# Optimization experiments

Hardware: AMD Instinct MI355X
Metric: run time of the kernel (lower is better)

Reference implementation:

```python
import jax, jax.numpy as jnp
import numpy as np

N_NODES = 50000


def _gcn_edges(edge_index, n):
    # add self loops, then symmetric GCN normalization D^-1/2 (A+I) D^-1/2
    loop = jnp.arange(n, dtype=edge_index.dtype)
    src = jnp.concatenate([edge_index[0], loop])
    dst = jnp.concatenate([edge_index[1], loop])
    deg = jax.ops.segment_sum(jnp.ones_like(src, dtype=jnp.float32), dst, num_segments=n)
    dinv = jnp.where(deg > 0, jax.lax.rsqrt(deg), 0.0)
    norm = dinv[src] * dinv[dst]
    return src, dst, norm


def _encoder(x, edge_index, w1, b1, w2, b2, w3, b3, n):
    src, dst, norm = _gcn_edges(edge_index, n)

    def prop(h):
        # sparse spmm: scatter-add of normalized gathered source features
        return jax.ops.segment_sum(h[src] * norm[:, None], dst, num_segments=n)

    def layer(h, w, b):
        # powers [0,1,2]: incrementally apply adjacency, linear per power, concat
        outs, cur = [], h
        for p in range(w.shape[0]):
            if p > 0:
                cur = prop(cur)
            outs.append(cur @ w[p] + b[p])
        return jnp.tanh(jnp.concatenate(outs, axis=-1))

    h = layer(x, w1, b1)
    h = layer(h, w2, b2)
    return layer(h, w3, b3)


def setup_inputs() -> dict:
    key = jax.random.key(0)
    ks = jax.random.split(key, 16)
    n, e, d = N_NODES, 800000, 256
    inp = {
        "x": jax.random.normal(ks[0], (n, d), dtype=jnp.float32),
        "edge_index": jax.random.randint(ks[1], (2, e), 0, n, dtype=jnp.int64),
    }
    dims = [(d, 64), (192, 64), (192, 64)]
    i = 2
    for enc in ("out", "in"):
        for li, (din, dout) in enumerate(dims, start=1):
            s = 1.0 / np.sqrt(din)
            inp[f"w{enc}{li}"] = jax.random.uniform(ks[i], (3, din, dout), jnp.float32, -s, s); i += 1
            inp[f"b{enc}{li}"] = jax.random.uniform(ks[i], (3, dout), jnp.float32, -s, s); i += 1
    return inp


def reference(x, edge_index, wout1, bout1, wout2, bout2, wout3, bout3,
              win1, bin1, win2, bin2, win3, bin3):
    n = x.shape[0]
    zout = _encoder(x, edge_index, wout1, bout1, wout2, bout2, wout3, bout3, n)
    zin = _encoder(x, edge_index[::-1], win1, bin1, win2, bin2, win3, bin3, n)
    return (zout, zin)
```

## Files before the change

### kernel.cpp

```cpp
#include <hip/hip_runtime.h>
#include <hip/hip_bf16.h>

#define NN 50000
#define EE 800000
#define NTILES 782
#define NB 391

typedef __bf16 bf16x8 __attribute__((ext_vector_type(8)));
typedef unsigned short us8 __attribute__((ext_vector_type(8)));
typedef float f32x4 __attribute__((ext_vector_type(4)));

__device__ __forceinline__ unsigned short f2bf(float f) {
  unsigned u = __float_as_uint(f);
  u += 0x7FFFu + ((u >> 16) & 1u);
  return (unsigned short)(u >> 16);
}
__device__ __forceinline__ float bflo(unsigned u) { return __uint_as_float(u << 16); }
__device__ __forceinline__ float bfhi(unsigned u) { return __uint_as_float(u & 0xFFFF0000u); }
__device__ __forceinline__ float bf2f(unsigned short h) { return __uint_as_float(((unsigned)h) << 16); }
__device__ __forceinline__ float fast_tanh(float x) {
  float e = __expf(2.0f * x);
  return 1.0f - 2.0f / (e + 1.0f);
}


__global__ __launch_bounds__(256) void k_hist(const int* __restrict__ ei, int* __restrict__ bCnt) {
  __shared__ int h[2 * NB];
  for (int i = threadIdx.x; i < 2 * NB; i += 256) h[i] = 0;
  __syncthreads();
  int base = blockIdx.x * 2048;
#pragma unroll
  for (int j = 0; j < 8; ++j) {
    int e = base + j * 256 + threadIdx.x;
    if (e < EE) {
      int s = ei[e], d = ei[EE + e];
      atomicAdd(&h[d >> 7], 1);
      atomicAdd(&h[NB + (s >> 7)], 1);
    }
  }
  __syncthreads();
  for (int i = threadIdx.x; i < 2 * NB; i += 256) {
    int c = h[i];
    if (c) atomicAdd(&bCnt[i], c);
  }
}

__global__ __launch_bounds__(512) void k_bscan(const int* __restrict__ bCnt,
                                               int* __restrict__ bOff, int* __restrict__ bCur) {
  __shared__ int sd[512];
  int z = blockIdx.x, t = threadIdx.x;
  sd[t] = (t < NB) ? bCnt[z * NB + t] : 0;
  __syncthreads();
  for (int o = 1; o < 512; o <<= 1) {
    int v = (t >= o) ? sd[t - o] : 0;
    __syncthreads();
    sd[t] += v;
    __syncthreads();
  }
  int ex = (t > 0) ? sd[t - 1] : 0;
  if (t < NB) { bOff[z * (NB + 1) + t] = ex; bCur[z * NB + t] = ex; }
  if (t == NB) bOff[z * (NB + 1) + NB] = ex;
}

__global__ __launch_bounds__(256) void k_scatter(const int* __restrict__ ei,
                                                 int* __restrict__ bCur,
                                                 unsigned* __restrict__ binA,
                                                 unsigned* __restrict__ binB) {
  __shared__ int h[2 * NB];
  for (int i = threadIdx.x; i < 2 * NB; i += 256) h[i] = 0;
  __syncthreads();
  int base = blockIdx.x * 2048;
  int s[8], d[8], la[8], lb[8];
#pragma unroll
  for (int j = 0; j < 8; ++j) {
    int e = base + j * 256 + threadIdx.x;
    d[j] = -1;
    if (e < EE) {
      s[j] = ei[e]; d[j] = ei[EE + e];
      la[j] = atomicAdd(&h[d[j] >> 7], 1);
      lb[j] = atomicAdd(&h[NB + (s[j] >> 7)], 1);
    }
  }
  __syncthreads();
  for (int i = threadIdx.x; i < 2 * NB; i += 256) {
    int c = h[i];
    if (c) h[i] = atomicAdd(&bCur[i], c);
  }
  __syncthreads();
#pragma unroll
  for (int j = 0; j < 8; ++j) {
    if (d[j] >= 0) {
      int pa = h[d[j] >> 7] + la[j];
      binA[pa] = ((unsigned)s[j] << 7) | (unsigned)(d[j] & 127);
      int pb = h[NB + (s[j] >> 7)] + lb[j];
      binB[pb] = ((unsigned)d[j] << 7) | (unsigned)(s[j] & 127);
    }
  }
}

__global__ __launch_bounds__(256) void k_build(const unsigned* __restrict__ binA,
                                               const unsigned* __restrict__ binB,
                                               const int* __restrict__ bOff,
                                               int* __restrict__ rpA, int* __restrict__ rpB,
                                               int* __restrict__ colA, int* __restrict__ colB,
                                               float* __restrict__ dinvA, float* __restrict__ dinvB) {
  int z = blockIdx.y, b = blockIdx.x, t = threadIdx.x;
  const unsigned* bin = z ? binB : binA;
  int* rp = z ? rpB : rpA;
  int* col = z ? colB : colA;
  float* dinv = z ? dinvB : dinvA;

  int e0 = bOff[z * (NB + 1) + b], e1 = bOff[z * (NB + 1) + b + 1];

  __shared__ int cnt[128];
  __shared__ int scn[128];
  __shared__ int cur[128];
  if (t < 128) cnt[t] = 0;
  __syncthreads();
  for (int e = e0 + t; e < e1; e += 256) atomicAdd(&cnt[bin[e] & 127], 1);
  __syncthreads();
  if (t < 128) scn[t] = cnt[t];
  __syncthreads();
  for (int o = 1; o < 128; o <<= 1) {
    int v = (t < 128 && t >= o) ? scn[t - o] : 0;
    __syncthreads();
    if (t < 128) scn[t] += v;
    __syncthreads();
  }
  if (t < 128) {
    int ex = scn[t] - cnt[t];
    cur[t] = ex;
    int node = b * 128 + t;
    if (node <= NN) rp[node] = e0 + ex;
    if (node < NN) dinv[node] = rsqrtf((float)(cnt[t] + 1));
  }
  __syncthreads();
  for (int e = e0 + t; e < e1; e += 256) {
    unsigned p = bin[e];
    int pos = e0 + atomicAdd(&cur[p & 127], 1);
    col[pos] = (int)(p >> 7);
  }
}


template<int K, bool F32IN>
__global__ __launch_bounds__(256) void k_gemm(const void* __restrict__ in0, const void* __restrict__ in1,
                                              const float* __restrict__ W0, const float* __restrict__ W1,
                                              unsigned short* __restrict__ Z0, unsigned short* __restrict__ Z1) {
  constexpr int KS = K / 32;
  constexpr int KP = K + 8;
  __shared__ unsigned short A_lds[64 * KP];

  int z = blockIdx.y;
  const void* Ain = z ? in1 : in0;
  const float* W = z ? W1 : W0;
  unsigned short* Zo = z ? Z1 : Z0;

  int t = threadIdx.x;
  int lane = t & 63, wv = t >> 6;
  int nloc = lane & 15, quad = lane >> 4;

  bf16x8 b[3][KS];
#pragma unroll
  for (int nt = 0; nt < 3; ++nt) {
    int ncol = wv * 48 + nt * 16 + nloc;
    const float* wp = W + (ncol >> 6) * (K * 64) + (ncol & 63);
#pragma unroll
    for (int ks = 0; ks < KS; ++ks) {
      int kb = ks * 32 + quad * 8;
      us8 u;
#pragma unroll
      for (int i = 0; i < 8; ++i) u[i] = f2bf(wp[(kb + i) * 64]);
      b[nt][ks] = __builtin_bit_cast(bf16x8, u);
    }
  }

  for (int bm = blockIdx.x; bm < NTILES; bm += gridDim.x) {
    int m0 = bm * 64;
    __syncthreads();
#pragma unroll
    for (int it = 0; it < KS; ++it) {
      int c = it * 256 + t;
      int row = c / (K / 8);
      int kc  = c % (K / 8);
      int gr = m0 + row;
      us8 val;
      if (F32IN) {
        float4 v0 = make_float4(0, 0, 0, 0), v1 = make_float4(0, 0, 0, 0);
        if (gr < NN) {
          const float* Af = (const float*)Ain + (size_t)gr * K + kc * 8;
          v0 = *(const float4*)(Af);
          v1 = *(const float4*)(Af + 4);
        }
        val[0] = f2bf(v0.x); val[1] = f2bf(v0.y); val[2] = f2bf(v0.z); val[3] = f2bf(v0.w);
        val[4] = f2bf(v1.x); val[5] = f2bf(v1.y); val[6] = f2bf(v1.z); val[7] = f2bf(v1.w);
      } else {
        if (gr < NN) val = *(const us8*)((const unsigned short*)Ain + (size_t)gr * K + kc * 8);
        else         val = (us8)0;
      }
      *(us8*)(&A_lds[row * KP + kc * 8]) = val;
    }
    __syncthreads();

    f32x4 acc[4][3];
#pragma unroll
    for (int mt = 0; mt < 4; ++mt)
#pragma unroll
      for (int nt = 0; nt < 3; ++nt) acc[mt][nt] = (f32x4){0.f, 0.f, 0.f, 0.f};

#pragma unroll
    for (int ks = 0; ks < KS; ++ks) {
      bf16x8 a[4];
#pragma unroll
      for (int mt = 0; mt < 4; ++mt)
        a[mt] = *(const bf16x8*)(&A_lds[(mt * 16 + nloc) * KP + ks * 32 + quad * 8]);
#pragma unroll
      for (int mt = 0; mt < 4; ++mt)
#pragma unroll
        for (int nt = 0; nt < 3; ++nt)
          acc[mt][nt] = __builtin_amdgcn_mfma_f32_16x16x32_bf16(a[mt], b[nt][ks], acc[mt][nt], 0, 0, 0);
    }

#pragma unroll
    for (int mt = 0; mt < 4; ++mt) {
      int rowb = m0 + mt * 16 + quad * 4;
#pragma unroll
      for (int nt = 0; nt < 3; ++nt) {
        int colg = wv * 48 + nt * 16 + nloc;
#pragma unroll
        for (int r = 0; r < 4; ++r) {
          int rr = rowb + r;
          if (rr < NN) Zo[(size_t)rr * 192 + colg] = f2bf(acc[mt][nt][r]);
        }
      }
    }
  }
}


__global__ __launch_bounds__(256) void k_prop1(const unsigned short* __restrict__ Z0,
                                               const unsigned short* __restrict__ Z1,
                                               unsigned short* __restrict__ T0,
                                               unsigned short* __restrict__ T1,
                                               const int* __restrict__ rpA, const int* __restrict__ rpB,
                                               const int* __restrict__ colA, const int* __restrict__ colB,
                                               const float* __restrict__ dinvA, const float* __restrict__ dinvB) {
  int z = blockIdx.y;
  const unsigned short* Z = z ? Z1 : Z0;
  unsigned short* T = z ? T1 : T0;
  const int* rp = z ? rpB : rpA;
  const int* col = z ? colB : colA;
  const float* dinv = z ? dinvB : dinvA;

  int wv = threadIdx.x >> 6, lane = threadIdx.x & 63;
  int v = blockIdx.x * 4 + wv;
  if (v >= NN) return;
  v = __builtin_amdgcn_readfirstlane(v);

  int e0 = rp[v], e1 = rp[v + 1];
  float dv = dinv[v];

  unsigned selfv = ((const unsigned*)(Z + (size_t)v * 192 + 64))[lane];
  float ax = bflo(selfv) * dv, ay = bfhi(selfv) * dv;

  int e = e0;
  for (; e + 2 <= e1; e += 2) {
    int s0 = col[e], s1 = col[e + 1];
    float d0 = dinv[s0], d1 = dinv[s1];
    unsigned p0 = ((const unsigned*)(Z + (size_t)s0 * 192 + 64))[lane];
    unsigned p1 = ((const unsigned*)(Z + (size_t)s1 * 192 + 64))[lane];
    ax += d0 * bflo(p0) + d1 * bflo(p1);
    ay += d0 * bfhi(p0) + d1 * bfhi(p1);
  }
  if (e < e1) {
    int s0 = col[e];
    float d0 = dinv[s0];
    unsigned p0 = ((const unsigned*)(Z + (size_t)s0 * 192 + 64))[lane];
    ax += d0 * bflo(p0);
    ay += d0 * bfhi(p0);
  }
  ax *= dv; ay *= dv;
  unsigned o = (unsigned)f2bf(ax) | ((unsigned)f2bf(ay) << 16);
  ((unsigned*)(T + (size_t)v * 128))[lane] = o;
}


template<bool FINAL>
__global__ __launch_bounds__(256) void k_combine(const unsigned short* __restrict__ Z0,
                                                 const unsigned short* __restrict__ Z1,
                                                 const unsigned short* __restrict__ T0,
                                                 const unsigned short* __restrict__ T1,
                                                 unsigned short* __restrict__ H0,
                                                 unsigned short* __restrict__ H1,
                                                 float* __restrict__ out,
                                                 const float* __restrict__ bia0, const float* __restrict__ bia1,
                                                 const int* __restrict__ rpA, const int* __restrict__ rpB,
                                                 const int* __restrict__ colA, const int* __restrict__ colB,
                                                 const float* __restrict__ dinvA, const float* __restrict__ dinvB) {
  int z = blockIdx.y;
  const unsigned short* Z = z ? Z1 : Z0;
  const unsigned short* T = z ? T1 : T0;
  unsigned short* H = z ? H1 : H0;
  const float* bias = z ? bia1 : bia0;
  const int* rp = z ? rpB : rpA;
  const int* col = z ? colB : colA;
  const float* dinv = z ? dinvB : dinvA;

  int wv = threadIdx.x >> 6, lane = threadIdx.x & 63;
  int v = blockIdx.x * 4 + wv;
  if (v >= NN) return;
  v = __builtin_amdgcn_readfirstlane(v);

  int e0 = rp[v], e1 = rp[v + 1];
  float dv = dinv[v];

  const unsigned short* Trow = T + (size_t)v * 128;
  float u = dv * bf2f(Trow[64 + lane]);

  int e = e0;
  for (; e + 2 <= e1; e += 2) {
    int s0 = col[e], s1 = col[e + 1];
    float d0 = dinv[s0], d1 = dinv[s1];
    float t0 = bf2f(T[(size_t)s0 * 128 + 64 + lane]);
    float t1 = bf2f(T[(size_t)s1 * 128 + 64 + lane]);
    u += d0 * t0 + d1 * t1;
  }
  if (e < e1) {
    int s0 = col[e];
    u += dinv[s0] * bf2f(T[(size_t)s0 * 128 + 64 + lane]);
  }
  u *= dv;

  float p0 = fast_tanh(bf2f(Z[(size_t)v * 192 + lane]) + bias[lane]);
  float p1 = fast_tanh(bf2f(Trow[lane]) + bias[64 + lane]);
  float p2 = fast_tanh(u + bias[128 + lane]);

  if (FINAL) {
    float* o = out + (size_t)z * NN * 192 + (size_t)v * 192;
    o[lane] = p0; o[lane + 64] = p1; o[lane + 128] = p2;
  } else {
    unsigned short* h = H + (size_t)v * 192;
    h[lane] = f2bf(p0); h[lane + 64] = f2bf(p1); h[lane + 128] = f2bf(p2);
  }
}


extern "C" void kernel_launch(void* const* d_in, const int* in_sizes, int n_in,
                              void* d_out, int out_size, void* d_ws, size_t ws_size,
                              hipStream_t stream) {
  const float* x  = (const float*)d_in[0];
  const int* ei   = (const int*)d_in[1];
  const float* wout1 = (const float*)d_in[2];
  const float* bout1 = (const float*)d_in[3];
  const float* wout2 = (const float*)d_in[4];
  const float* bout2 = (const float*)d_in[5];
  const float* wout3 = (const float*)d_in[6];
  const float* bout3 = (const float*)d_in[7];
  const float* win1  = (const float*)d_in[8];
  const float* bin1  = (const float*)d_in[9];
  const float* win2  = (const float*)d_in[10];
  const float* bin2  = (const float*)d_in[11];
  const float* win3  = (const float*)d_in[12];
  const float* bin3  = (const float*)d_in[13];
  float* out = (float*)d_out;

  char* p = (char*)d_ws;
  auto alloc = [&](size_t bytes) { char* r = p; p += (bytes + 255) & ~(size_t)255; return r; };
  int* rpA   = (int*)alloc((size_t)(NN + 1) * 4);
  int* rpB   = (int*)alloc((size_t)(NN + 1) * 4);
  int* colA  = (int*)alloc((size_t)EE * 4);
  int* colB  = (int*)alloc((size_t)EE * 4);
  float* dinvA = (float*)alloc((size_t)NN * 4);
  float* dinvB = (float*)alloc((size_t)NN * 4);
  int* bCnt  = (int*)alloc((size_t)2 * NB * 4);
  int* bOff  = (int*)alloc((size_t)2 * (NB + 1) * 4);
  int* bCur  = (int*)alloc((size_t)2 * NB * 4);
  unsigned short* Z0 = (unsigned short*)alloc((size_t)NN * 192 * 2);
  unsigned short* Z1 = (unsigned short*)alloc((size_t)NN * 192 * 2);
  unsigned short* T0 = (unsigned short*)alloc((size_t)NN * 128 * 2);
  unsigned short* T1 = (unsigned short*)alloc((size_t)NN * 128 * 2);
  unsigned short* H0 = (unsigned short*)alloc((size_t)NN * 192 * 2);
  unsigned short* H1 = (unsigned short*)alloc((size_t)NN * 192 * 2);

  unsigned* binA = (unsigned*)Z0;
  unsigned* binB = (unsigned*)Z1;

  hipMemsetAsync(bCnt, 0, (size_t)2 * NB * 4, stream);
  k_hist<<<391, 256, 0, stream>>>(ei, bCnt);
  k_bscan<<<2, 512, 0, stream>>>(bCnt, bOff, bCur);
  k_scatter<<<391, 256, 0, stream>>>(ei, bCur, binA, binB);
  k_build<<<dim3(NB, 2), 256, 0, stream>>>(binA, binB, bOff, rpA, rpB, colA, colB, dinvA, dinvB);

  dim3 gGemm(196, 2);
  dim3 gProp(12500, 2);

  k_gemm<256, true><<<gGemm, 256, 0, stream>>>(x, x, wout1, win1, Z0, Z1);
  k_prop1<<<gProp, 256, 0, stream>>>(Z0, Z1, T0, T1, rpA, rpB, colA, colB, dinvA, dinvB);
  k_combine<false><<<gProp, 256, 0, stream>>>(Z0, Z1, T0, T1, H0, H1, nullptr, bout1, bin1,
                                              rpA, rpB, colA, colB, dinvA, dinvB);
  k_gemm<192, false><<<gGemm, 256, 0, stream>>>(H0, H1, wout2, win2, Z0, Z1);
  k_prop1<<<gProp, 256, 0, stream>>>(Z0, Z1, T0, T1, rpA, rpB, colA, colB, dinvA, dinvB);
  k_combine<false><<<gProp, 256, 0, stream>>>(Z0, Z1, T0, T1, H0, H1, nullptr, bout2, bin2,
                                              rpA, rpB, colA, colB, dinvA, dinvB);
  k_gemm<192, false><<<gGemm, 256, 0, stream>>>(H0, H1, wout3, win3, Z0, Z1);
  k_prop1<<<gProp, 256, 0, stream>>>(Z0, Z1, T0, T1, rpA, rpB, colA, colB, dinvA, dinvB);
  k_combine<true><<<gProp, 256, 0, stream>>>(Z0, Z1, T0, T1, H0, H1, out, bout3, bin3,
                                             rpA, rpB, colA, colB, dinvA, dinvB);
}
```

Before: 688.2 us.

## Prescale gathered features by source dinv and batch edge gathers by eight

The GEMM epilogue now multiplies the propagated columns by each row's dinv, and prop1 writes its second-hop half prescaled by dinv as well. The SpMM loops then just sum neighbor rows, with no per-edge dinv gather or multiply. The gather loops are also unrolled to eight edges with the next batch of column indices prefetched, so more loads are in flight. The col arrays get eight padding entries so the tail batch can read past the end, and the early return on v >= NN was removed (the grid divides evenly). Rounding changes slightly because the scaled values are stored in bf16.

```diff
diff --git a/kernel.cpp b/kernel.cpp
--- a/kernel.cpp
+++ b/kernel.cpp
@@ -134,6 +134,7 @@
     if (node <= NN) rp[node] = e0 + ex;
     if (node < NN) dinv[node] = rsqrtf((float)(cnt[t] + 1));
   }
+  if (b == 0 && t < 8) col[EE + t] = 0;
   __syncthreads();
   for (int e = e0 + t; e < e1; e += 256) {
     unsigned p = bin[e];
@@ -146,14 +147,17 @@
 template<int K, bool F32IN>
 __global__ __launch_bounds__(256) void k_gemm(const void* __restrict__ in0, const void* __restrict__ in1,
                                               const float* __restrict__ W0, const float* __restrict__ W1,
+                                              const float* __restrict__ dinvA, const float* __restrict__ dinvB,
                                               unsigned short* __restrict__ Z0, unsigned short* __restrict__ Z1) {
   constexpr int KS = K / 32;
   constexpr int KP = K + 8;
   __shared__ unsigned short A_lds[64 * KP];
+  __shared__ float dvt[64];
 
   int z = blockIdx.y;
   const void* Ain = z ? in1 : in0;
   const float* W = z ? W1 : W0;
+  const float* dinv = z ? dinvB : dinvA;
   unsigned short* Zo = z ? Z1 : Z0;
 
   int t = threadIdx.x;
@@ -178,6 +182,7 @@
   for (int bm = blockIdx.x; bm < NTILES; bm += gridDim.x) {
     int m0 = bm * 64;
     __syncthreads();
+    if (t < 64) dvt[t] = (m0 + t < NN) ? dinv[m0 + t] : 0.f;
 #pragma unroll
     for (int it = 0; it < KS; ++it) {
       int c = it * 256 + t;
@@ -227,10 +232,12 @@
 #pragma unroll
       for (int nt = 0; nt < 3; ++nt) {
         int colg = wv * 48 + nt * 16 + nloc;
+        bool sc = (wv * 48 + nt * 16) >= 64;
 #pragma unroll
         for (int r = 0; r < 4; ++r) {
           int rr = rowb + r;
-          if (rr < NN) Zo[(size_t)rr * 192 + colg] = f2bf(acc[mt][nt][r]);
+          float scale = sc ? dvt[mt * 16 + quad * 4 + r] : 1.0f;
+          if (rr < NN) Zo[(size_t)rr * 192 + colg] = f2bf(acc[mt][nt][r] * scale);
         }
       }
     }
@@ -254,33 +261,53 @@
 
   int wv = threadIdx.x >> 6, lane = threadIdx.x & 63;
   int v = blockIdx.x * 4 + wv;
-  if (v >= NN) return;
   v = __builtin_amdgcn_readfirstlane(v);
 
   int e0 = rp[v], e1 = rp[v + 1];
   float dv = dinv[v];
 
   unsigned selfv = ((const unsigned*)(Z + (size_t)v * 192 + 64))[lane];
-  float ax = bflo(selfv) * dv, ay = bfhi(selfv) * dv;
+  float ax = bflo(selfv), ay = bfhi(selfv);
 
   int e = e0;
-  for (; e + 2 <= e1; e += 2) {
-    int s0 = col[e], s1 = col[e + 1];
-    float d0 = dinv[s0], d1 = dinv[s1];
-    unsigned p0 = ((const unsigned*)(Z + (size_t)s0 * 192 + 64))[lane];
-    unsigned p1 = ((const unsigned*)(Z + (size_t)s1 * 192 + 64))[lane];
-    ax += d0 * bflo(p0) + d1 * bflo(p1);
-    ay += d0 * bfhi(p0) + d1 * bfhi(p1);
-  }
-  if (e < e1) {
-    int s0 = col[e];
-    float d0 = dinv[s0];
-    unsigned p0 = ((const unsigned*)(Z + (size_t)s0 * 192 + 64))[lane];
-    ax += d0 * bflo(p0);
-    ay += d0 * bfhi(p0);
-  }
+  if (e + 8 <= e1) {
+    int idx[8];
+#pragma unroll
+    for (int j = 0; j < 8; ++j) idx[j] = col[e + j];
+    e += 8;
+    for (; e + 8 <= e1; e += 8) {
+      int nidx[8];
+#pragma unroll
+      for (int j = 0; j < 8; ++j) nidx[j] = col[e + j];
+      unsigned pp[8];
+#pragma unroll
+      for (int j = 0; j < 8; ++j) pp[j] = ((const unsigned*)(Z + (size_t)idx[j] * 192 + 64))[lane];
+#pragma unroll
+      for (int j = 0; j < 8; ++j) { ax += bflo(pp[j]); ay += bfhi(pp[j]); }
+#pragma unroll
+      for (int j = 0; j < 8; ++j) idx[j] = nidx[j];
+    }
+    unsigned pp[8];
+#pragma unroll
+    for (int j = 0; j < 8; ++j) pp[j] = ((const unsigned*)(Z + (size_t)idx[j] * 192 + 64))[lane];
+#pragma unroll
+    for (int j = 0; j < 8; ++j) { ax += bflo(pp[j]); ay += bfhi(pp[j]); }
+  }
+  int r = e1 - e;
+  if (r > 0) {
+    int idx[8];
+#pragma unroll
+    for (int j = 0; j < 8; ++j) idx[j] = col[e + j];
+    unsigned pp[8];
+#pragma unroll
+    for (int j = 0; j < 8; ++j) pp[j] = ((const unsigned*)(Z + (size_t)idx[j] * 192 + 64))[lane];
+#pragma unroll
+    for (int j = 0; j < 8; ++j) if (j < r) { ax += bflo(pp[j]); ay += bfhi(pp[j]); }
+  }
+
   ax *= dv; ay *= dv;
-  unsigned o = (unsigned)f2bf(ax) | ((unsigned)f2bf(ay) << 16);
+  float sc = (lane >= 32) ? dv : 1.0f;
+  unsigned o = (unsigned)f2bf(ax * sc) | ((unsigned)f2bf(ay * sc) << 16);
   ((unsigned*)(T + (size_t)v * 128))[lane] = o;
 }
 
@@ -308,26 +335,48 @@
 
   int wv = threadIdx.x >> 6, lane = threadIdx.x & 63;
   int v = blockIdx.x * 4 + wv;
-  if (v >= NN) return;
   v = __builtin_amdgcn_readfirstlane(v);
 
   int e0 = rp[v], e1 = rp[v + 1];
   float dv = dinv[v];
 
   const unsigned short* Trow = T + (size_t)v * 128;
-  float u = dv * bf2f(Trow[64 + lane]);
+  float u = bf2f(Trow[64 + lane]);
 
   int e = e0;
-  for (; e + 2 <= e1; e += 2) {
-    int s0 = col[e], s1 = col[e + 1];
-    float d0 = dinv[s0], d1 = dinv[s1];
-    float t0 = bf2f(T[(size_t)s0 * 128 + 64 + lane]);
-    float t1 = bf2f(T[(size_t)s1 * 128 + 64 + lane]);
-    u += d0 * t0 + d1 * t1;
-  }
-  if (e < e1) {
-    int s0 = col[e];
-    u += dinv[s0] * bf2f(T[(size_t)s0 * 128 + 64 + lane]);
+  if (e + 8 <= e1) {
+    int idx[8];
+#pragma unroll
+    for (int j = 0; j < 8; ++j) idx[j] = col[e + j];
+    e += 8;
+    for (; e + 8 <= e1; e += 8) {
+      int nidx[8];
+#pragma unroll
+      for (int j = 0; j < 8; ++j) nidx[j] = col[e + j];
+      float pp[8];
+#pragma unroll
+      for (int j = 0; j < 8; ++j) pp[j] = bf2f(T[(size_t)idx[j] * 128 + 64 + lane]);
+#pragma unroll
+      for (int j = 0; j < 8; ++j) u += pp[j];
+#pragma unroll
+      for (int j = 0; j < 8; ++j) idx[j] = nidx[j];
+    }
+    float pp[8];
+#pragma unroll
+    for (int j = 0; j < 8; ++j) pp[j] = bf2f(T[(size_t)idx[j] * 128 + 64 + lane]);
+#pragma unroll
+    for (int j = 0; j < 8; ++j) u += pp[j];
+  }
+  int r = e1 - e;
+  if (r > 0) {
+    int idx[8];
+#pragma unroll
+    for (int j = 0; j < 8; ++j) idx[j] = col[e + j];
+    float pp[8];
+#pragma unroll
+    for (int j = 0; j < 8; ++j) pp[j] = bf2f(T[(size_t)idx[j] * 128 + 64 + lane]);
+#pragma unroll
+    for (int j = 0; j < 8; ++j) if (j < r) u += pp[j];
   }
   u *= dv;
 
@@ -368,8 +417,8 @@
   auto alloc = [&](size_t bytes) { char* r = p; p += (bytes + 255) & ~(size_t)255; return r; };
   int* rpA   = (int*)alloc((size_t)(NN + 1) * 4);
   int* rpB   = (int*)alloc((size_t)(NN + 1) * 4);
-  int* colA  = (int*)alloc((size_t)EE * 4);
-  int* colB  = (int*)alloc((size_t)EE * 4);
+  int* colA  = (int*)alloc((size_t)(EE + 8) * 4);
+  int* colB  = (int*)alloc((size_t)(EE + 8) * 4);
   float* dinvA = (float*)alloc((size_t)NN * 4);
   float* dinvB = (float*)alloc((size_t)NN * 4);
   int* bCnt  = (int*)alloc((size_t)2 * NB * 4);
@@ -394,15 +443,15 @@
   dim3 gGemm(196, 2);
   dim3 gProp(12500, 2);
 
-  k_gemm<256, true><<<gGemm, 256, 0, stream>>>(x, x, wout1, win1, Z0, Z1);
+  k_gemm<256, true><<<gGemm, 256, 0, stream>>>(x, x, wout1, win1, dinvA, dinvB, Z0, Z1);
   k_prop1<<<gProp, 256, 0, stream>>>(Z0, Z1, T0, T1, rpA, rpB, colA, colB, dinvA, dinvB);
   k_combine<false><<<gProp, 256, 0, stream>>>(Z0, Z1, T0, T1, H0, H1, nullptr, bout1, bin1,
                                               rpA, rpB, colA, colB, dinvA, dinvB);
-  k_gemm<192, false><<<gGemm, 256, 0, stream>>>(H0, H1, wout2, win2, Z0, Z1);
+  k_gemm<192, false><<<gGemm, 256, 0, stream>>>(H0, H1, wout2, win2, dinvA, dinvB, Z0, Z1);
   k_prop1<<<gProp, 256, 0, stream>>>(Z0, Z1, T0, T1, rpA, rpB, colA, colB, dinvA, dinvB);
   k_combine<false><<<gProp, 256, 0, stream>>>(Z0, Z1, T0, T1, H0, H1, nullptr, bout2, bin2,
                                               rpA, rpB, colA, colB, dinvA, dinvB);
-  k_gemm<192, false><<<gGemm, 256, 0, stream>>>(H0, H1, wout3, win3, Z0, Z1);
+  k_gemm<192, false><<<gGemm, 256, 0, stream>>>(H0, H1, wout3, win3, dinvA, dinvB, Z0, Z1);
   k_prop1<<<gProp, 256, 0, stream>>>(Z0, Z1, T0, T1, rpA, rpB, colA, colB, dinvA, dinvB);
   k_combine<true><<<gProp, 256, 0, stream>>>(Z0, Z1, T0, T1, H0, H1, out, bout3, bin3,
                                              rpA, rpB, colA, colB, dinvA, dinvB);
```

Measured after the change: 565.4 us. 1.22x faster.
